# Kernel optimization log

Measured on AMD Instinct MI355X. Metric: run time of the kernel, lower is better.

The kernel has to match this reference:

```python
import jax, jax.numpy as jnp
import numpy as np

B, T, D, H, L, K, DFF = 8, 512, 512, 8, 4, 31, 2048
DK = D // H
PAD = (K - 1) // 2

def _ln(x, g, b, eps=1e-5):
    m = x.mean(-1, keepdims=True)
    v = ((x - m) ** 2).mean(-1, keepdims=True)
    return (x - m) * jax.lax.rsqrt(v + eps) * g + b

def _swish(x):
    return x * jax.nn.sigmoid(x)

def _rel_shift(x):
    # x: [B,H,T,P] with P = 2T-1 (Transformer-XL style shift)
    b, h, q, p = x.shape
    x = jnp.pad(x, ((0, 0), (0, 0), (0, 0), (1, 0)))
    x = x.reshape(b, h, p + 1, q)[:, :, 1:].reshape(b, h, q, p)
    return x

def setup_inputs() -> dict:
    key = jax.random.key(0)
    ks = iter(jax.random.split(key, 64))
    def w(shape, s=0.02):
        return jax.random.normal(next(ks), shape, jnp.float32) * s
    inp = {
        'x': jax.random.normal(next(ks), (B, T, D), jnp.float32),
        'pos_emb': jax.random.normal(next(ks), (1, 2 * T - 1, D), jnp.float32),
        'ln1_g': jnp.ones((L, D)), 'ln1_b': jnp.zeros((L, D)),
        'ff1_w1': w((L, D, DFF)), 'ff1_b1': jnp.zeros((L, DFF)),
        'ff1_w2': w((L, DFF, D)), 'ff1_b2': jnp.zeros((L, D)),
        'lnA_g': jnp.ones((L, D)), 'lnA_b': jnp.zeros((L, D)),
        'Wq': w((L, D, D)), 'bq': jnp.zeros((L, D)),
        'Wk': w((L, D, D)), 'bk': jnp.zeros((L, D)),
        'Wv': w((L, D, D)), 'bv': jnp.zeros((L, D)),
        'Wo': w((L, D, D)), 'bo': jnp.zeros((L, D)),
        'Wpos': w((L, D, D)),
        'pbu': jnp.zeros((L, H, DK)), 'pbv': jnp.zeros((L, H, DK)),
        'lnC_g': jnp.ones((L, D)), 'lnC_b': jnp.zeros((L, D)),
        'pw1_w': w((L, 2 * D, D)), 'pw1_b': jnp.zeros((L, 2 * D)),
        'dw_w': w((L, D, K)), 'dw_b': jnp.zeros((L, D)),
        'cln_g': jnp.ones((L, D)), 'cln_b': jnp.zeros((L, D)),
        'pw2_w': w((L, D, D)), 'pw2_b': jnp.zeros((L, D)),
        'ln2_g': jnp.ones((L, D)), 'ln2_b': jnp.zeros((L, D)),
        'ff2_w1': w((L, D, DFF)), 'ff2_b1': jnp.zeros((L, DFF)),
        'ff2_w2': w((L, DFF, D)), 'ff2_b2': jnp.zeros((L, D)),
        'lnO_g': jnp.ones((L, D)), 'lnO_b': jnp.zeros((L, D)),
    }
    return inp

def reference(x, pos_emb, ln1_g, ln1_b, ff1_w1, ff1_b1, ff1_w2, ff1_b2,
              lnA_g, lnA_b, Wq, bq, Wk, bk, Wv, bv, Wo, bo, Wpos, pbu, pbv,
              lnC_g, lnC_b, pw1_w, pw1_b, dw_w, dw_b, cln_g, cln_b, pw2_w, pw2_b,
              ln2_g, ln2_b, ff2_w1, ff2_b1, ff2_w2, ff2_b2, lnO_g, lnO_b):
    scale = 1.0 / np.sqrt(DK).astype(np.float32)
    for i in range(L):
        # FFN 1 (half-step residual)
        res = x
        y = _ln(x, ln1_g[i], ln1_b[i])
        y = _swish(y @ ff1_w1[i] + ff1_b1[i]) @ ff1_w2[i] + ff1_b2[i]
        res = res + 0.5 * y
        # rel-pos multi-head self-attention
        y = _ln(res, lnA_g[i], lnA_b[i])
        q = (y @ Wq[i] + bq[i]).reshape(B, T, H, DK)
        k = (y @ Wk[i] + bk[i]).reshape(B, T, H, DK)
        v = (y @ Wv[i] + bv[i]).reshape(B, T, H, DK)
        p = (pos_emb @ Wpos[i]).reshape(1, 2 * T - 1, H, DK)
        ac = jnp.einsum('bthd,bshd->bhts', q + pbu[i], k)          # content score
        bd = jnp.einsum('bthd,xshd->bhts', q + pbv[i], p)          # position score
        bd = _rel_shift(bd)[..., :T]
        attn = jax.nn.softmax((ac + bd) * scale, axis=-1)
        o = jnp.einsum('bhts,bshd->bthd', attn, v).reshape(B, T, D)
        res = res + (o @ Wo[i] + bo[i])
        # convolution module
        y = _ln(res, lnC_g[i], lnC_b[i])
        y = y @ pw1_w[i].T + pw1_b[i]                               # (B,T,2D)
        a, g = jnp.split(y, 2, axis=-1)
        y = a * jax.nn.sigmoid(g)                                   # GLU over channels
        y = jax.lax.conv_general_dilated(
            y.transpose(0, 2, 1), dw_w[i][:, None, :],
            window_strides=(1,), padding=[(PAD, PAD)],
            feature_group_count=D,
            dimension_numbers=('NCH', 'OIH', 'NCH'))
        y = y.transpose(0, 2, 1) + dw_b[i]                          # (B,T,D)
        y = _swish(_ln(y, cln_g[i], cln_b[i]))
        y = y @ pw2_w[i].T + pw2_b[i]
        res = res + y
        # FFN 2 (half-step residual)
        y = _ln(res, ln2_g[i], ln2_b[i])
        y = _swish(y @ ff2_w1[i] + ff2_b1[i]) @ ff2_w2[i] + ff2_b2[i]
        res = res + 0.5 * y
        x = _ln(res, lnO_g[i], lnO_b[i])
    return x
```

## Files before the change

kernel.cpp:

```cpp
#include <hip/hip_runtime.h>


typedef unsigned short u16;
typedef unsigned int u32;
typedef __attribute__((ext_vector_type(8))) short bf16x8;
typedef __attribute__((ext_vector_type(4))) float f32x4;

#define DI __device__ __forceinline__

constexpr int CT = 512;
constexpr int CD = 512;
constexpr int CH = 8;
constexpr int CDK = 64;
constexpr int CDFF = 2048;
constexpr int CNBT = 4096;
constexpr int CL = 4;

DI u16 f2bf(float f) {
  u32 u = __builtin_bit_cast(u32, f);
  u = u + 0x7fffu + ((u >> 16) & 1u);
  return (u16)(u >> 16);
}
DI float bf2f(u16 h) { u32 u = ((u32)h) << 16; return __builtin_bit_cast(float, u); }
DI u32 pack2(float a, float b) { return (u32)f2bf(a) | ((u32)f2bf(b) << 16); }
DI float sigm(float x) { return 1.0f / (1.0f + __expf(-x)); }

DI f32x4 MFMA(bf16x8 a, bf16x8 b, f32x4 c) {
  return __builtin_amdgcn_mfma_f32_16x16x32_bf16(a, b, c, 0, 0, 0);
}

DI void gload16(const void* g, void* l) {
  __builtin_amdgcn_global_load_lds((const __attribute__((address_space(1))) void*)g,
                                   (__attribute__((address_space(3))) void*)l, 16, 0, 0);
}

DI float wsum(float v) {
#pragma unroll
  for (int o = 32; o > 0; o >>= 1) v += __shfl_xor(v, o, 64);
  return v;
}

DI void tbody(const float* ip, u16* op, int R, int C, int c0, int r0,
              int tx, int ty) {
  __shared__ float t[32][33];
#pragma unroll
  for (int i = ty; i < 32; i += 8)
    t[i][tx] = ip[(long)(r0 + i) * C + c0 + tx];
  __syncthreads();
#pragma unroll
  for (int i = ty; i < 32; i += 8)
    op[(long)(c0 + i) * R + r0 + tx] = f2bf(t[tx][i]);
}

__global__ __launch_bounds__(256) void tconv2x_k(const float* __restrict__ in0,
                                                 const float* __restrict__ in1,
                                                 u16* __restrict__ out0,
                                                 u16* __restrict__ out1,
                                                 int R, int C) {
  int z = blockIdx.z;
  int l = z & 3;
  const float* ip = (z < 4 ? in0 : in1) + (long)l * R * C;
  u16* op = (z < 4 ? out0 : out1) + (long)l * R * C;
  tbody(ip, op, R, C, blockIdx.x * 32, blockIdx.y * 32, threadIdx.x, threadIdx.y);
}

__global__ __launch_bounds__(256) void tconvQ_k(
    const float* __restrict__ Wq, const float* __restrict__ Wk,
    const float* __restrict__ Wv, const float* __restrict__ Wo,
    const float* __restrict__ Wpos, u16* __restrict__ wt_qkv,
    u16* __restrict__ wt_o, u16* __restrict__ wt_pos) {
  int z = blockIdx.z;
  int sel = z >> 2, l = z & 3;
  const float* ip;
  u16* op;
  const long S = 512L * 512;
  switch (sel) {
    case 0: ip = Wq + l * S; op = wt_qkv + (long)l * 1536 * 512; break;
    case 1: ip = Wk + l * S; op = wt_qkv + (long)l * 1536 * 512 + S; break;
    case 2: ip = Wv + l * S; op = wt_qkv + (long)l * 1536 * 512 + 2 * S; break;
    case 3: ip = Wo + l * S; op = wt_o + l * S; break;
    default: ip = Wpos + l * S; op = wt_pos + l * S; break;
  }
  tbody(ip, op, 512, 512, blockIdx.x * 32, blockIdx.y * 32, threadIdx.x, threadIdx.y);
}

__global__ __launch_bounds__(256) void cvt_k(const float* __restrict__ in,
                                             u16* __restrict__ out, long nIn, long nOut,
                                             long inZ, long outZ) {
  long i = ((long)blockIdx.x * 256 + threadIdx.x) * 4;
  if (i >= nOut) return;
  const float* ip = in + (long)blockIdx.y * inZ;
  u16* op = out + (long)blockIdx.y * outZ;
  u16 o[4];
#pragma unroll
  for (int j = 0; j < 4; ++j) {
    long idx = i + j;
    o[j] = (idx < nIn) ? f2bf(ip[idx]) : (u16)0;
  }
  uint2 st;
  st.x = (u32)o[0] | ((u32)o[1] << 16);
  st.y = (u32)o[2] | ((u32)o[3] << 16);
  *(uint2*)&op[i] = st;
}

__global__ __launch_bounds__(256) void pwperm_k(const float* __restrict__ in,
                                                u16* __restrict__ out) {
  int l = blockIdx.y;
  long i = (long)blockIdx.x * 256 + threadIdx.x;
  long n = i >> 7;
  int c = (int)(i & 127) * 4;
  int q = (int)(n >> 4) & 1;
  long r = (q ? 512 : 0) + ((n >> 5) << 4) + (n & 15);
  const float* ip = in + ((long)l * 1024 + r) * 512 + c;
  float4 v = *(const float4*)ip;
  u16* op = out + ((long)l * 1024 + n) * 512 + c;
  uint2 st;
  st.x = pack2(v.x, v.y);
  st.y = pack2(v.z, v.w);
  *(uint2*)op = st;
}

__global__ __launch_bounds__(256) void dwt_k(const float* __restrict__ in,
                                             float* __restrict__ out) {
  int l = blockIdx.y;
  int idx = blockIdx.x * 256 + threadIdx.x;
  if (idx >= 512 * 31) return;
  int k = idx >> 9, d = idx & 511;
  out[(long)l * 31 * 512 + idx] = in[(long)l * 512 * 31 + d * 31 + k];
}

__global__ __launch_bounds__(256) void qkvbias_k(const float* __restrict__ bq,
                                                 const float* __restrict__ bk,
                                                 const float* __restrict__ bv,
                                                 float* __restrict__ out) {
  int z = blockIdx.y;
  int j = blockIdx.x * 256 + threadIdx.x;
  float v;
  if (j < 512) v = bq[z * 512 + j];
  else if (j < 1024) v = bk[z * 512 + j - 512];
  else v = bv[z * 512 + j - 1024];
  out[z * 1536 + j] = v;
}

__global__ __launch_bounds__(256) void copy_k(const float* __restrict__ in,
                                              float* __restrict__ out) {
  long i = ((long)blockIdx.x * 256 + threadIdx.x) * 4;
  *(float4*)(out + i) = *(const float4*)(in + i);
}

template <int F32OUT>
__global__ __launch_bounds__(256) void ln_k(const float* in, void* out,
                                            const float* gw, const float* bw) {
  int tid = threadIdx.x, wid = tid >> 6, lane = tid & 63;
  long row = (long)blockIdx.x * 4 + wid;
  const float* x = in + row * CD + lane * 8;
  float4 v0 = *(const float4*)x;
  float4 v1 = *(const float4*)(x + 4);
  float s = v0.x + v0.y + v0.z + v0.w + v1.x + v1.y + v1.z + v1.w;
  float q = v0.x * v0.x + v0.y * v0.y + v0.z * v0.z + v0.w * v0.w +
            v1.x * v1.x + v1.y * v1.y + v1.z * v1.z + v1.w * v1.w;
  s = wsum(s);
  q = wsum(q);
  float mean = s * (1.0f / CD);
  float var = q * (1.0f / CD) - mean * mean;
  float rs = rsqrtf(var + 1e-5f);
  int c = lane * 8;
  float4 g0 = *(const float4*)(gw + c), g1 = *(const float4*)(gw + c + 4);
  float4 b0 = *(const float4*)(bw + c), b1 = *(const float4*)(bw + c + 4);
  float y0 = (v0.x - mean) * rs * g0.x + b0.x;
  float y1 = (v0.y - mean) * rs * g0.y + b0.y;
  float y2 = (v0.z - mean) * rs * g0.z + b0.z;
  float y3 = (v0.w - mean) * rs * g0.w + b0.w;
  float y4 = (v1.x - mean) * rs * g1.x + b1.x;
  float y5 = (v1.y - mean) * rs * g1.y + b1.y;
  float y6 = (v1.z - mean) * rs * g1.z + b1.z;
  float y7 = (v1.w - mean) * rs * g1.w + b1.w;
  if (F32OUT) {
    float* o = (float*)out + row * CD + c;
    *(float4*)o = make_float4(y0, y1, y2, y3);
    *(float4*)(o + 4) = make_float4(y4, y5, y6, y7);
  } else {
    u16* o = (u16*)out + row * CD + c;
    uint4 pk;
    pk.x = pack2(y0, y1);
    pk.y = pack2(y2, y3);
    pk.z = pack2(y4, y5);
    pk.w = pack2(y6, y7);
    *(uint4*)o = pk;
  }
}

__global__ __launch_bounds__(256) void lnln_k(float* cur, u16* ybf,
                                              const float* gO, const float* bO,
                                              const float* g1, const float* b1) {
  int tid = threadIdx.x, wid = tid >> 6, lane = tid & 63;
  long row = (long)blockIdx.x * 4 + wid;
  float* x = cur + row * CD + lane * 8;
  float v[8];
  *(float4*)&v[0] = *(const float4*)x;
  *(float4*)&v[4] = *(const float4*)(x + 4);
  float s = 0.f, q = 0.f;
#pragma unroll
  for (int j = 0; j < 8; ++j) { s += v[j]; q += v[j] * v[j]; }
  s = wsum(s);
  q = wsum(q);
  float mean = s * (1.0f / CD);
  float var = q * (1.0f / CD) - mean * mean;
  float rs = rsqrtf(var + 1e-5f);
  int c = lane * 8;
  float y[8];
#pragma unroll
  for (int j = 0; j < 8; ++j) y[j] = (v[j] - mean) * rs * gO[c + j] + bO[c + j];
  *(float4*)x = *(float4*)&y[0];
  *(float4*)(x + 4) = *(float4*)&y[4];
  float s2 = 0.f, q2 = 0.f;
#pragma unroll
  for (int j = 0; j < 8; ++j) { s2 += y[j]; q2 += y[j] * y[j]; }
  s2 = wsum(s2);
  q2 = wsum(q2);
  float mean2 = s2 * (1.0f / CD);
  float var2 = q2 * (1.0f / CD) - mean2 * mean2;
  float rs2 = rsqrtf(var2 + 1e-5f);
  float z[8];
#pragma unroll
  for (int j = 0; j < 8; ++j) z[j] = (y[j] - mean2) * rs2 * g1[c + j] + b1[c + j];
  u16* o = ybf + row * CD + c;
  uint4 pk;
  pk.x = pack2(z[0], z[1]);
  pk.y = pack2(z[2], z[3]);
  pk.z = pack2(z[4], z[5]);
  pk.w = pack2(z[6], z[7]);
  *(uint4*)o = pk;
}

template <int EPI, int SPLITK>
__global__ __launch_bounds__(256, 2) void gemm2_k(
    const u16* __restrict__ A, const u16* __restrict__ B, void* C,
    u16* __restrict__ Caux,
    const float* __restrict__ bias, float alpha, int lda, int ldb, int ldc, int Kd) {
  __shared__ u16 lds[2][2][64 * 64];
  const int tid = threadIdx.x, wid = tid >> 6, lane = tid & 63;
  const int m0 = blockIdx.x * 64, n0 = blockIdx.y * 64;
  const int wm = wid >> 1, wn = wid & 1;
  const int fr = lane & 15, fq = lane >> 4;
  const f32x4 vz = {0.f, 0.f, 0.f, 0.f};
  f32x4 acc[2][2] = {{vz, vz}, {vz, vz}};

  const int Kc = Kd / SPLITK;
  const int kb0 = (SPLITK > 1) ? blockIdx.z * Kc : 0;
  const int nK = Kc / 64;

  auto stage = [&](int buf, int kt) {
    const int k0 = kb0 + kt * 64;
#pragma unroll
    for (int r = 0; r < 2; ++r) {
      int bi = r * 4096 + tid * 16;
      int row = bi >> 7;
      int ch = ((bi >> 4) & 7) ^ (row & 7);
      gload16(A + (long)(m0 + row) * lda + k0 + ch * 8,
              (char*)&lds[buf][0][0] + r * 4096 + wid * 1024);
      gload16(B + (long)(n0 + row) * ldb + k0 + ch * 8,
              (char*)&lds[buf][1][0] + r * 4096 + wid * 1024);
    }
  };

  stage(0, 0);
  asm volatile("s_waitcnt vmcnt(0)" ::: "memory");
  __syncthreads();
  int buf = 0;
  for (int kt = 0; kt < nK; ++kt) {
    if (kt + 1 < nK) stage(buf ^ 1, kt + 1);
    bf16x8 af[2][2], bfv[2][2];
#pragma unroll
    for (int ks = 0; ks < 2; ++ks) {
      int ch = ks * 4 + fq;
#pragma unroll
      for (int i = 0; i < 2; ++i) {
        int arow = wm * 32 + i * 16 + fr;
        af[ks][i] = *(const bf16x8*)((const char*)&lds[buf][0][0] + arow * 128 +
                                     ((ch ^ (arow & 7)) << 4));
        int brow = wn * 32 + i * 16 + fr;
        bfv[ks][i] = *(const bf16x8*)((const char*)&lds[buf][1][0] + brow * 128 +
                                      ((ch ^ (brow & 7)) << 4));
      }
    }
#pragma unroll
    for (int ks = 0; ks < 2; ++ks)
#pragma unroll
      for (int mi = 0; mi < 2; ++mi)
#pragma unroll
        for (int ni = 0; ni < 2; ++ni)
          acc[mi][ni] = MFMA(af[ks][mi], bfv[ks][ni], acc[mi][ni]);
    asm volatile("s_waitcnt vmcnt(0)" ::: "memory");
    __syncthreads();
    buf ^= 1;
  }

  if constexpr (EPI == 7) {
    const int ucol = (n0 >> 1) + wn * 16 + fr;
    float ba = bias[ucol], bg = bias[512 + ucol];
#pragma unroll
    for (int mi = 0; mi < 2; ++mi) {
      const int gmB = m0 + wm * 32 + mi * 16 + fq * 4;
#pragma unroll
      for (int r = 0; r < 4; ++r) {
        float va = acc[mi][0][r] + ba;
        float vg = acc[mi][1][r] + bg;
        ((u16*)C)[(long)(gmB + r) * 512 + ucol] = f2bf(va * sigm(vg));
      }
    }
  } else if constexpr (EPI == 8) {
    if (n0 < 1024) {
#pragma unroll
      for (int mi = 0; mi < 2; ++mi) {
        const int gmB = m0 + wm * 32 + mi * 16 + fq * 4;
#pragma unroll
        for (int ni = 0; ni < 2; ++ni) {
          const int gn = n0 + wn * 32 + ni * 16 + fr;
          float bv_ = bias[gn];
#pragma unroll
          for (int r = 0; r < 4; ++r)
            ((u16*)C)[(long)(gmB + r) * ldc + gn] = f2bf(acc[mi][ni][r] + bv_);
        }
      }
    } else {
#pragma unroll
      for (int mi = 0; mi < 2; ++mi) {
        const int gmB = m0 + wm * 32 + mi * 16 + fq * 4;
        const int b = gmB >> 9, t = gmB & 511;
#pragma unroll
        for (int ni = 0; ni < 2; ++ni) {
          const int gn = n0 + wn * 32 + ni * 16 + fr;
          const int h = (gn - 1024) >> 6, d = (gn - 1024) & 63;
          float bv_ = bias[gn];
          uint2 pk;
          pk.x = pack2(acc[mi][ni][0] + bv_, acc[mi][ni][1] + bv_);
          pk.y = pack2(acc[mi][ni][2] + bv_, acc[mi][ni][3] + bv_);
          *(uint2*)&Caux[((long)(b * 8 + h) * 64 + d) * 512 + t] = pk;
        }
      }
    }
  } else {
#pragma unroll
    for (int mi = 0; mi < 2; ++mi) {
      const int gmB = m0 + wm * 32 + mi * 16 + fq * 4;
#pragma unroll
      for (int ni = 0; ni < 2; ++ni) {
        const int gn = n0 + wn * 32 + ni * 16 + fr;
        float bv_ = 0.f;
        if constexpr (EPI == 1 || EPI == 2 || EPI == 3) bv_ = bias[gn];
#pragma unroll
        for (int r = 0; r < 4; ++r) {
          const int gm = gmB + r;
          float v = acc[mi][ni][r];
          long idx = (long)gm * ldc + gn;
          if constexpr (EPI == 0) ((u16*)C)[idx] = f2bf(v);
          else if constexpr (EPI == 1) ((u16*)C)[idx] = f2bf(v + bv_);
          else if constexpr (EPI == 2) {
            float x = v + bv_;
            ((u16*)C)[idx] = f2bf(x * sigm(x));
          } else if constexpr (EPI == 3) {
            float* R = (float*)C;
            if constexpr (SPLITK > 1) {
              float add = alpha * (v + (blockIdx.z == 0 ? bv_ : 0.f));
              atomicAdd(&R[idx], add);
            } else {
              R[idx] += alpha * (v + bv_);
            }
          }
        }
      }
    }
  }
}

__global__ __launch_bounds__(256, 2) void attn_k(
    const u16* __restrict__ qkvp, const u16* __restrict__ pball,
    const float* __restrict__ pbuL, const float* __restrict__ pbvL,
    const u16* __restrict__ vt, u16* __restrict__ out) {
  __shared__ u16 ldsK[2][64 * 64];
  __shared__ u16 ldsP[2][128 * 64];
  __shared__ u16 bd0s[4][16 * 80];
  __shared__ u16 stile[4][16 * 64];
  const int tid = threadIdx.x, wid = tid >> 6, lane = tid & 63;
  const int t0 = blockIdx.x * 64;
  const int bh = blockIdx.y, b = bh >> 3, h = bh & 7;
  const int fr = lane & 15, fq = lane >> 4;

  const u16* kbase = qkvp + (long)(b * CT) * 1536 + 512 + h * 64;
  const u16* pbase = pball + h * 64;
  const float* pu = pbuL + h * 64;
  const float* pv = pbvL + h * 64;

  const u16* qp = qkvp + (long)(b * CT + t0 + wid * 16 + fr) * 1536 + h * 64;
  bf16x8 qua[2], qva[2];
#pragma unroll
  for (int kk = 0; kk < 2; ++kk) {
    bf16x8 qw = *(const bf16x8*)(qp + kk * 32 + fq * 8);
    const float* bu = pu + kk * 32 + fq * 8;
    const float* bv = pv + kk * 32 + fq * 8;
#pragma unroll
    for (int j = 0; j < 8; ++j) {
      float qf = bf2f((u16)qw[j]);
      qua[kk][j] = (short)f2bf(qf + bu[j]);
      qva[kk][j] = (short)f2bf(qf + bv[j]);
    }
  }

  const f32x4 vz = {0.f, 0.f, 0.f, 0.f};
  f32x4 oacc[4] = {vz, vz, vz, vz};
  float m_run[4] = {-1e30f, -1e30f, -1e30f, -1e30f};
  float l_run[4] = {0.f, 0.f, 0.f, 0.f};
  const int jbw = (3 - wid) * 16;

  auto stage = [&](int buf, int st) {
    int s0 = st * 64, j0 = s0 - t0 + 448;
#pragma unroll
    for (int r = 0; r < 2; ++r) {
      int c = r * 256 + tid;
      int row = c >> 3, cs = (c & 7) ^ (row & 7);
      gload16(kbase + (long)(s0 + row) * 1536 + cs * 8,
              (char*)&ldsK[buf][0] + r * 4096 + wid * 1024);
    }
#pragma unroll
    for (int r = 0; r < 4; ++r) {
      int c = r * 256 + tid;
      int row = c >> 3, cs = (c & 7) ^ (row & 7);
      gload16(pbase + (long)(j0 + row) * 2048 + cs * 8,
              (char*)&ldsP[buf][0] + r * 4096 + wid * 1024);
    }
  };

  stage(0, 0);
  int cur = 0;
  for (int st = 0; st < 8; ++st) {
    const int s0 = st * 64;
    if (st + 1 < 8) {
      stage(cur ^ 1, st + 1);
      asm volatile("s_waitcnt vmcnt(6)" ::: "memory");
    } else {
      asm volatile("s_waitcnt vmcnt(0)" ::: "memory");
    }
    __syncthreads();

    bf16x8 vb[4][2];
#pragma unroll
    for (int ni = 0; ni < 4; ++ni)
#pragma unroll
      for (int kk = 0; kk < 2; ++kk)
        vb[ni][kk] = *(const bf16x8*)&vt[((long)bh * 64 + ni * 16 + fr) * 512 +
                                         s0 + kk * 32 + fq * 8];

    f32x4 ac[4] = {vz, vz, vz, vz};
#pragma unroll
    for (int kk = 0; kk < 2; ++kk) {
#pragma unroll
      for (int ni = 0; ni < 4; ++ni) {
        int row = ni * 16 + fr;
        bf16x8 kb = *(const bf16x8*)((const char*)&ldsK[cur][0] +
                                     ((row * 128 + kk * 64 + fq * 16) ^ ((row & 7) << 4)));
        ac[ni] = MFMA(qua[kk], kb, ac[ni]);
      }
    }
    f32x4 bd[5] = {vz, vz, vz, vz, vz};
#pragma unroll
    for (int kk = 0; kk < 2; ++kk) {
#pragma unroll
      for (int nbi = 0; nbi < 5; ++nbi) {
        int row = jbw + nbi * 16 + fr;
        bf16x8 pb = *(const bf16x8*)((const char*)&ldsP[cur][0] +
                                     ((row * 128 + kk * 64 + fq * 16) ^ ((row & 7) << 4)));
        bd[nbi] = MFMA(qva[kk], pb, bd[nbi]);
      }
    }
#pragma unroll
    for (int nbi = 0; nbi < 5; ++nbi)
#pragma unroll
      for (int r = 0; r < 4; ++r)
        bd0s[wid][(fq * 4 + r) * 80 + nbi * 16 + fr] = f2bf(bd[nbi][r]);

    float vals[4][4];
#pragma unroll
    for (int ni = 0; ni < 4; ++ni)
#pragma unroll
      for (int r = 0; r < 4; ++r) {
        int tlw = fq * 4 + r;
        int jcol = ni * 16 + fr + 15 - tlw;
        vals[ni][r] = (ac[ni][r] + bf2f(bd0s[wid][tlw * 80 + jcol])) * 0.125f;
      }
    float scf[4];
#pragma unroll
    for (int r = 0; r < 4; ++r) {
      float mx = fmaxf(fmaxf(vals[0][r], vals[1][r]), fmaxf(vals[2][r], vals[3][r]));
      mx = fmaxf(mx, __shfl_xor(mx, 1));
      mx = fmaxf(mx, __shfl_xor(mx, 2));
      mx = fmaxf(mx, __shfl_xor(mx, 4));
      mx = fmaxf(mx, __shfl_xor(mx, 8));
      float mnew = fmaxf(m_run[r], mx);
      scf[r] = __expf(m_run[r] - mnew);
      m_run[r] = mnew;
      float sum = 0.f;
#pragma unroll
      for (int ni = 0; ni < 4; ++ni) {
        float p = __expf(vals[ni][r] - mnew);
        vals[ni][r] = p;
        sum += p;
      }
      sum += __shfl_xor(sum, 1);
      sum += __shfl_xor(sum, 2);
      sum += __shfl_xor(sum, 4);
      sum += __shfl_xor(sum, 8);
      l_run[r] = l_run[r] * scf[r] + sum;
    }
#pragma unroll
    for (int ni = 0; ni < 4; ++ni)
#pragma unroll
      for (int r = 0; r < 4; ++r) {
        int tlw = fq * 4 + r;
        *(u16*)((char*)&stile[wid][0] +
                (((tlw * 128) + (ni * 16 + fr) * 2) ^ ((tlw & 7) << 4))) =
            f2bf(vals[ni][r]);
      }
#pragma unroll
    for (int ni = 0; ni < 4; ++ni)
#pragma unroll
      for (int r = 0; r < 4; ++r) oacc[ni][r] *= scf[r];
#pragma unroll
    for (int kk = 0; kk < 2; ++kk) {
      bf16x8 pa = *(const bf16x8*)((const char*)&stile[wid][0] +
                                   ((fr * 128 + kk * 64 + fq * 16) ^ ((fr & 7) << 4)));
#pragma unroll
      for (int ni = 0; ni < 4; ++ni) oacc[ni] = MFMA(pa, vb[ni][kk], oacc[ni]);
    }
    __syncthreads();
    cur ^= 1;
  }

  float inv[4];
#pragma unroll
  for (int r = 0; r < 4; ++r) inv[r] = 1.0f / l_run[r];
#pragma unroll
  for (int ni = 0; ni < 4; ++ni)
#pragma unroll
    for (int r = 0; r < 4; ++r) {
      long row = (long)(b * CT + t0 + wid * 16 + fq * 4 + r) * CD + h * CDK;
      out[row + ni * 16 + fr] = f2bf(oacc[ni][r] * inv[r]);
    }
}

__global__ __launch_bounds__(256) void conv2_k(const u16* __restrict__ u,
                                               const float* __restrict__ wT,
                                               const float* __restrict__ wb,
                                               const float* __restrict__ cg,
                                               const float* __restrict__ cb,
                                               u16* __restrict__ out) {
  constexpr int TT = 8;
  int tid = threadIdx.x, d0 = tid * 2;
  int b = blockIdx.y, t0 = blockIdx.x * TT;
  const u16* ub = u + ((long)b * CT) * CD + d0;

  u32 strip[TT + 30];
#pragma unroll
  for (int j = 0; j < TT + 30; ++j) {
    int tt = t0 + j - 15;
    strip[j] = ((unsigned)tt < (unsigned)CT) ? *(const u32*)(ub + (long)tt * CD) : 0u;
  }
  float2 bias = *(const float2*)(wb + d0);
  float a0[TT], a1[TT];
#pragma unroll
  for (int t = 0; t < TT; ++t) { a0[t] = bias.x; a1[t] = bias.y; }
#pragma unroll
  for (int k = 0; k < 31; ++k) {
    float2 wk = *(const float2*)(wT + k * CD + d0);
#pragma unroll
    for (int t = 0; t < TT; ++t) {
      u32 pr = strip[t + k];
      a0[t] += bf2f((u16)(pr & 0xffff)) * wk.x;
      a1[t] += bf2f((u16)(pr >> 16)) * wk.y;
    }
  }
  __shared__ float redS[4][TT], redQ[4][TT];
  int wid = tid >> 6, lane = tid & 63;
#pragma unroll
  for (int t = 0; t < TT; ++t) {
    float s = a0[t] + a1[t];
    float q = a0[t] * a0[t] + a1[t] * a1[t];
    s = wsum(s);
    q = wsum(q);
    if (lane == 0) { redS[wid][t] = s; redQ[wid][t] = q; }
  }
  __syncthreads();
  float2 g2 = *(const float2*)(cg + d0);
  float2 b2 = *(const float2*)(cb + d0);
#pragma unroll
  for (int t = 0; t < TT; ++t) {
    float s = redS[0][t] + redS[1][t] + redS[2][t] + redS[3][t];
    float q = redQ[0][t] + redQ[1][t] + redQ[2][t] + redQ[3][t];
    float mean = s * (1.f / 512), var = q * (1.f / 512) - mean * mean;
    float rs = rsqrtf(var + 1e-5f);
    float y0 = (a0[t] - mean) * rs * g2.x + b2.x;
    float y1 = (a1[t] - mean) * rs * g2.y + b2.y;
    y0 = y0 * sigm(y0);
    y1 = y1 * sigm(y1);
    *(u32*)(out + ((long)(b * CT + t0 + t)) * CD + d0) = pack2(y0, y1);
  }
}

extern "C" void kernel_launch(void* const* d_in, const int* in_sizes, int n_in,
                              void* d_out, int out_size, void* d_ws, size_t ws_size,
                              hipStream_t stream) {
  const float* in_x   = (const float*)d_in[0];
  const float* in_pos = (const float*)d_in[1];
  const float* ln1_g  = (const float*)d_in[2];
  const float* ln1_b  = (const float*)d_in[3];
  const float* ff1_w1 = (const float*)d_in[4];
  const float* ff1_b1 = (const float*)d_in[5];
  const float* ff1_w2 = (const float*)d_in[6];
  const float* ff1_b2 = (const float*)d_in[7];
  const float* lnA_g  = (const float*)d_in[8];
  const float* lnA_b  = (const float*)d_in[9];
  const float* Wq     = (const float*)d_in[10];
  const float* bq     = (const float*)d_in[11];
  const float* Wk     = (const float*)d_in[12];
  const float* bk     = (const float*)d_in[13];
  const float* Wv     = (const float*)d_in[14];
  const float* bv     = (const float*)d_in[15];
  const float* Wo     = (const float*)d_in[16];
  const float* bo     = (const float*)d_in[17];
  const float* Wpos   = (const float*)d_in[18];
  const float* pbu    = (const float*)d_in[19];
  const float* pbv    = (const float*)d_in[20];
  const float* lnC_g  = (const float*)d_in[21];
  const float* lnC_b  = (const float*)d_in[22];
  const float* pw1_w  = (const float*)d_in[23];
  const float* pw1_b  = (const float*)d_in[24];
  const float* dw_w   = (const float*)d_in[25];
  const float* dw_b   = (const float*)d_in[26];
  const float* cln_g  = (const float*)d_in[27];
  const float* cln_b  = (const float*)d_in[28];
  const float* pw2_w  = (const float*)d_in[29];
  const float* pw2_b  = (const float*)d_in[30];
  const float* ln2_g  = (const float*)d_in[31];
  const float* ln2_b  = (const float*)d_in[32];
  const float* ff2_w1 = (const float*)d_in[33];
  const float* ff2_b1 = (const float*)d_in[34];
  const float* ff2_w2 = (const float*)d_in[35];
  const float* ff2_b2 = (const float*)d_in[36];
  const float* lnO_g  = (const float*)d_in[37];
  const float* lnO_b  = (const float*)d_in[38];
  (void)in_sizes; (void)n_in; (void)out_size; (void)ws_size;

  char* ws = (char*)d_ws;
  size_t off = 0;
  auto alloc = [&](size_t bytes) -> void* {
    off = (off + 255) & ~(size_t)255;
    void* p = ws + off;
    off += bytes;
    return p;
  };

  u16* wt_ff1w1 = (u16*)alloc((size_t)CL * CDFF * CD * 2);
  u16* wt_ff1w2 = (u16*)alloc((size_t)CL * CD * CDFF * 2);
  u16* wt_qkv   = (u16*)alloc((size_t)CL * 1536 * CD * 2);
  u16* wt_o     = (u16*)alloc((size_t)CL * CD * CD * 2);
  u16* wt_pos   = (u16*)alloc((size_t)CL * CD * CD * 2);
  u16* w_pw1p   = (u16*)alloc((size_t)CL * 1024 * CD * 2);
  u16* w_pw2    = (u16*)alloc((size_t)CL * CD * CD * 2);
  u16* wt_ff2w1 = (u16*)alloc((size_t)CL * CDFF * CD * 2);
  u16* wt_ff2w2 = (u16*)alloc((size_t)CL * CD * CDFF * 2);
  float* qkvbias = (float*)alloc((size_t)CL * 1536 * 4);
  u16* posbf = (u16*)alloc((size_t)1024 * CD * 2);
  float* dwT = (float*)alloc((size_t)CL * 31 * CD * 4);
  u16* pbf_all = (u16*)alloc((size_t)1024 * 2048 * 2);
  float* cur = (float*)alloc((size_t)CNBT * CD * 4);
  u16* ybf   = (u16*)alloc((size_t)CNBT * CD * 2);
  u16* qkv   = (u16*)alloc((size_t)CNBT * 1536 * 2);
  u16* hbf   = (u16*)alloc((size_t)CNBT * CDFF * 2);
  u16* vt    = (u16*)alloc((size_t)64 * CDK * CT * 2);
  u16* obf   = (u16*)alloc((size_t)CNBT * CD * 2);
  u16* ubuf  = (u16*)alloc((size_t)CNBT * CD * 2);
  u16* cbf   = (u16*)alloc((size_t)CNBT * CD * 2);

  dim3 b256(256);
  dim3 tb(32, 8);

  tconv2x_k<<<dim3(CDFF / 32, CD / 32, 2 * CL), tb, 0, stream>>>(
      ff1_w1, ff2_w1, wt_ff1w1, wt_ff2w1, CD, CDFF);
  tconv2x_k<<<dim3(CD / 32, CDFF / 32, 2 * CL), tb, 0, stream>>>(
      ff1_w2, ff2_w2, wt_ff1w2, wt_ff2w2, CDFF, CD);
  tconvQ_k<<<dim3(CD / 32, CD / 32, 5 * CL), tb, 0, stream>>>(
      Wq, Wk, Wv, Wo, Wpos, wt_qkv, wt_o, wt_pos);
  pwperm_k<<<dim3(512, CL), b256, 0, stream>>>(pw1_w, w_pw1p);
  cvt_k<<<dim3(256, CL, 1), b256, 0, stream>>>(pw2_w, w_pw2, 512L * 512, 512L * 512,
                                               512L * 512, 512L * 512);
  cvt_k<<<dim3(512, 1, 1), b256, 0, stream>>>(in_pos, posbf, 1023L * 512, 1024L * 512, 0, 0);
  dwt_k<<<dim3(62, CL), b256, 0, stream>>>(dw_w, dwT);
  qkvbias_k<<<dim3(6, CL), b256, 0, stream>>>(bq, bk, bv, qkvbias);
  copy_k<<<dim3(2048), b256, 0, stream>>>(in_x, cur);
  gemm2_k<0, 1><<<dim3(16, 32, 1), b256, 0, stream>>>(
      posbf, wt_pos, pbf_all, nullptr, nullptr, 0.f, CD, CD, 2048, CD);
  ln_k<0><<<dim3(1024), b256, 0, stream>>>(cur, ybf, ln1_g, ln1_b);

  for (int i = 0; i < CL; ++i) {
    const u16* Wf1 = wt_ff1w1 + (long)i * CDFF * CD;
    const u16* Wf2 = wt_ff1w2 + (long)i * CD * CDFF;
    const u16* Wqk = wt_qkv + (long)i * 1536 * CD;
    const u16* Wou = wt_o + (long)i * CD * CD;
    const u16* Wp1 = w_pw1p + (long)i * 1024 * CD;
    const u16* Wp2 = w_pw2 + (long)i * CD * CD;
    const u16* Wf3 = wt_ff2w1 + (long)i * CDFF * CD;
    const u16* Wf4 = wt_ff2w2 + (long)i * CD * CDFF;

    gemm2_k<2, 1><<<dim3(64, 32, 1), b256, 0, stream>>>(
        ybf, Wf1, hbf, nullptr, ff1_b1 + (long)i * CDFF, 0.f, CD, CD, CDFF, CD);
    gemm2_k<3, 2><<<dim3(64, 8, 2), b256, 0, stream>>>(
        hbf, Wf2, cur, nullptr, ff1_b2 + i * CD, 0.5f, CDFF, CDFF, CD, CDFF);

    ln_k<0><<<dim3(1024), b256, 0, stream>>>(cur, ybf, lnA_g + i * CD, lnA_b + i * CD);
    gemm2_k<8, 1><<<dim3(64, 24, 1), b256, 0, stream>>>(
        ybf, Wqk, qkv, vt, qkvbias + i * 1536, 0.f, CD, CD, 1536, CD);
    attn_k<<<dim3(8, 64), b256, 0, stream>>>(qkv, pbf_all + i * 512, pbu + i * 512,
                                             pbv + i * 512, vt, obf);
    gemm2_k<3, 1><<<dim3(64, 8, 1), b256, 0, stream>>>(
        obf, Wou, cur, nullptr, bo + i * CD, 1.0f, CD, CD, CD, CD);

    ln_k<0><<<dim3(1024), b256, 0, stream>>>(cur, ybf, lnC_g + i * CD, lnC_b + i * CD);
    gemm2_k<7, 1><<<dim3(64, 16, 1), b256, 0, stream>>>(
        ybf, Wp1, ubuf, nullptr, pw1_b + (long)i * 1024, 0.f, CD, CD, 512, CD);
    conv2_k<<<dim3(CT / 8, 8), b256, 0, stream>>>(ubuf, dwT + (long)i * 31 * CD,
                                                  dw_b + i * CD, cln_g + i * CD,
                                                  cln_b + i * CD, cbf);
    gemm2_k<3, 1><<<dim3(64, 8, 1), b256, 0, stream>>>(
        cbf, Wp2, cur, nullptr, pw2_b + i * CD, 1.0f, CD, CD, CD, CD);

    ln_k<0><<<dim3(1024), b256, 0, stream>>>(cur, ybf, ln2_g + i * CD, ln2_b + i * CD);
    gemm2_k<2, 1><<<dim3(64, 32, 1), b256, 0, stream>>>(
        ybf, Wf3, hbf, nullptr, ff2_b1 + (long)i * CDFF, 0.f, CD, CD, CDFF, CD);
    gemm2_k<3, 2><<<dim3(64, 8, 2), b256, 0, stream>>>(
        hbf, Wf4, cur, nullptr, ff2_b2 + i * CD, 0.5f, CDFF, CDFF, CD, CDFF);

    if (i < CL - 1)
      lnln_k<<<dim3(1024), b256, 0, stream>>>(cur, ybf, lnO_g + i * CD, lnO_b + i * CD,
                                              ln1_g + (i + 1) * CD, ln1_b + (i + 1) * CD);
    else
      ln_k<1><<<dim3(1024), b256, 0, stream>>>(cur, d_out, lnO_g + i * CD, lnO_b + i * CD);
  }
}
```

Before: 794.8 us.

## Add 128x128-tile GEMM for wide projections and fuse setup kernels

Adds a gemmB_k kernel with 128x128 output tiles (each wave computing 4x4 MFMA fragments). It is used for the FFN up-projections, the fused QKV projection and the GLU pointwise conv, replacing the 64x64-tile GEMM there to get more operand reuse per LDS load and fewer blocks. The setup kernels (pos conversion, dw transpose, qkv bias) are merged into one launch, and the input copy is fused with the first layernorm. The larger tiles raise register and LDS pressure and cut the number of blocks, which may reduce occupancy and CU fill on the smaller GEMMs.

```diff
diff --git a/kernel.cpp b/kernel.cpp
--- a/kernel.cpp
+++ b/kernel.cpp
@@ -120,32 +120,45 @@
   *(uint2*)op = st;
 }
 
-__global__ __launch_bounds__(256) void dwt_k(const float* __restrict__ in,
-                                             float* __restrict__ out) {
-  int l = blockIdx.y;
-  int idx = blockIdx.x * 256 + threadIdx.x;
-  if (idx >= 512 * 31) return;
-  int k = idx >> 9, d = idx & 511;
-  out[(long)l * 31 * 512 + idx] = in[(long)l * 512 * 31 + d * 31 + k];
-}
-
-__global__ __launch_bounds__(256) void qkvbias_k(const float* __restrict__ bq,
-                                                 const float* __restrict__ bk,
-                                                 const float* __restrict__ bv,
-                                                 float* __restrict__ out) {
-  int z = blockIdx.y;
-  int j = blockIdx.x * 256 + threadIdx.x;
-  float v;
-  if (j < 512) v = bq[z * 512 + j];
-  else if (j < 1024) v = bk[z * 512 + j - 512];
-  else v = bv[z * 512 + j - 1024];
-  out[z * 1536 + j] = v;
-}
-
-__global__ __launch_bounds__(256) void copy_k(const float* __restrict__ in,
-                                              float* __restrict__ out) {
-  long i = ((long)blockIdx.x * 256 + threadIdx.x) * 4;
-  *(float4*)(out + i) = *(const float4*)(in + i);
+__global__ __launch_bounds__(256) void setup3_k(
+    const float* __restrict__ in_pos, u16* __restrict__ posbf,
+    const float* __restrict__ dw_w, float* __restrict__ dwT,
+    const float* __restrict__ bq, const float* __restrict__ bk,
+    const float* __restrict__ bv, float* __restrict__ qkvb) {
+  int y = blockIdx.y;
+  long x = blockIdx.x;
+  int tid = threadIdx.x;
+  if (y == 0) {
+    long i = (x * 256 + tid) * 4;
+    const long nIn = 1023L * 512, nOut = 1024L * 512;
+    if (i >= nOut) return;
+    u16 o[4];
+#pragma unroll
+    for (int j = 0; j < 4; ++j) {
+      long idx = i + j;
+      o[j] = (idx < nIn) ? f2bf(in_pos[idx]) : (u16)0;
+    }
+    uint2 st;
+    st.x = (u32)o[0] | ((u32)o[1] << 16);
+    st.y = (u32)o[2] | ((u32)o[3] << 16);
+    *(uint2*)&posbf[i] = st;
+  } else if (y == 1) {
+    long idx = x * 256 + tid;
+    if (idx >= 4L * 31 * 512) return;
+    long l = idx / (31 * 512);
+    int rem = (int)(idx % (31 * 512));
+    int k = rem >> 9, d = rem & 511;
+    dwT[idx] = dw_w[l * 512 * 31 + d * 31 + k];
+  } else {
+    long idx = x * 256 + tid;
+    if (idx >= 4L * 1536) return;
+    int z = (int)(idx / 1536), j = (int)(idx % 1536);
+    float v;
+    if (j < 512) v = bq[z * 512 + j];
+    else if (j < 1024) v = bk[z * 512 + j - 512];
+    else v = bv[z * 512 + j - 1024];
+    qkvb[idx] = v;
+  }
 }
 
 template <int F32OUT>
@@ -190,6 +203,40 @@
   }
 }
 
+__global__ __launch_bounds__(256) void ln_cp_k(const float* __restrict__ in,
+                                               float* __restrict__ cur,
+                                               u16* __restrict__ ybf,
+                                               const float* gw, const float* bw) {
+  int tid = threadIdx.x, wid = tid >> 6, lane = tid & 63;
+  long row = (long)blockIdx.x * 4 + wid;
+  const float* x = in + row * CD + lane * 8;
+  float v[8];
+  *(float4*)&v[0] = *(const float4*)x;
+  *(float4*)&v[4] = *(const float4*)(x + 4);
+  float* cx = cur + row * CD + lane * 8;
+  *(float4*)cx = *(float4*)&v[0];
+  *(float4*)(cx + 4) = *(float4*)&v[4];
+  float s = 0.f, q = 0.f;
+#pragma unroll
+  for (int j = 0; j < 8; ++j) { s += v[j]; q += v[j] * v[j]; }
+  s = wsum(s);
+  q = wsum(q);
+  float mean = s * (1.0f / CD);
+  float var = q * (1.0f / CD) - mean * mean;
+  float rs = rsqrtf(var + 1e-5f);
+  int c = lane * 8;
+  float y[8];
+#pragma unroll
+  for (int j = 0; j < 8; ++j) y[j] = (v[j] - mean) * rs * gw[c + j] + bw[c + j];
+  u16* o = ybf + row * CD + c;
+  uint4 pk;
+  pk.x = pack2(y[0], y[1]);
+  pk.y = pack2(y[2], y[3]);
+  pk.z = pack2(y[4], y[5]);
+  pk.w = pack2(y[6], y[7]);
+  *(uint4*)o = pk;
+}
+
 __global__ __launch_bounds__(256) void lnln_k(float* cur, u16* ybf,
                                               const float* gO, const float* bO,
                                               const float* g1, const float* b1) {
@@ -236,7 +283,6 @@
 template <int EPI, int SPLITK>
 __global__ __launch_bounds__(256, 2) void gemm2_k(
     const u16* __restrict__ A, const u16* __restrict__ B, void* C,
-    u16* __restrict__ Caux,
     const float* __restrict__ bias, float alpha, int lda, int ldb, int ldc, int Kd) {
   __shared__ u16 lds[2][2][64 * 64];
   const int tid = threadIdx.x, wid = tid >> 6, lane = tid & 63;
@@ -296,27 +342,136 @@
     buf ^= 1;
   }
 
-  if constexpr (EPI == 7) {
-    const int ucol = (n0 >> 1) + wn * 16 + fr;
-    float ba = bias[ucol], bg = bias[512 + ucol];
-#pragma unroll
-    for (int mi = 0; mi < 2; ++mi) {
-      const int gmB = m0 + wm * 32 + mi * 16 + fq * 4;
+#pragma unroll
+  for (int mi = 0; mi < 2; ++mi) {
+    const int gmB = m0 + wm * 32 + mi * 16 + fq * 4;
+#pragma unroll
+    for (int ni = 0; ni < 2; ++ni) {
+      const int gn = n0 + wn * 32 + ni * 16 + fr;
+      float bv_ = 0.f;
+      if constexpr (EPI == 3) bv_ = bias[gn];
 #pragma unroll
       for (int r = 0; r < 4; ++r) {
-        float va = acc[mi][0][r] + ba;
-        float vg = acc[mi][1][r] + bg;
-        ((u16*)C)[(long)(gmB + r) * 512 + ucol] = f2bf(va * sigm(vg));
+        const int gm = gmB + r;
+        float v = acc[mi][ni][r];
+        long idx = (long)gm * ldc + gn;
+        if constexpr (EPI == 0) ((u16*)C)[idx] = f2bf(v);
+        else if constexpr (EPI == 3) {
+          float* R = (float*)C;
+          if constexpr (SPLITK > 1) {
+            float add = alpha * (v + (blockIdx.z == 0 ? bv_ : 0.f));
+            atomicAdd(&R[idx], add);
+          } else {
+            R[idx] += alpha * (v + bv_);
+          }
+        }
+      }
+    }
+  }
+}
+
+template <int EPI>
+__global__ __launch_bounds__(256, 2) void gemmB_k(
+    const u16* __restrict__ A, const u16* __restrict__ B, void* C,
+    u16* __restrict__ Caux, const float* __restrict__ bias,
+    int lda, int ldb, int ldc, int Kd) {
+  __shared__ u16 ldsA[2][128 * 64];
+  __shared__ u16 ldsB[2][128 * 64];
+  const int tid = threadIdx.x, wid = tid >> 6, lane = tid & 63;
+  const int m0 = blockIdx.x * 128, n0 = blockIdx.y * 128;
+  const int wm = wid >> 1, wn = wid & 1;
+  const int fr = lane & 15, fq = lane >> 4;
+  const f32x4 vz = {0.f, 0.f, 0.f, 0.f};
+  f32x4 acc[4][4];
+#pragma unroll
+  for (int mi = 0; mi < 4; ++mi)
+#pragma unroll
+    for (int ni = 0; ni < 4; ++ni) acc[mi][ni] = vz;
+  const int nK = Kd / 64;
+
+  auto stage = [&](int buf, int kt) {
+    const int k0 = kt * 64;
+#pragma unroll
+    for (int r = 0; r < 4; ++r) {
+      int bi = r * 4096 + tid * 16;
+      int row = bi >> 7;
+      int ch = ((bi >> 4) & 7) ^ (row & 7);
+      gload16(A + (long)(m0 + row) * lda + k0 + ch * 8,
+              (char*)&ldsA[buf][0] + r * 4096 + wid * 1024);
+      gload16(B + (long)(n0 + row) * ldb + k0 + ch * 8,
+              (char*)&ldsB[buf][0] + r * 4096 + wid * 1024);
+    }
+  };
+
+  stage(0, 0);
+  asm volatile("s_waitcnt vmcnt(0)" ::: "memory");
+  __syncthreads();
+  int buf = 0;
+  for (int kt = 0; kt < nK; ++kt) {
+    if (kt + 1 < nK) stage(buf ^ 1, kt + 1);
+#pragma unroll
+    for (int ks = 0; ks < 2; ++ks) {
+      int ch = ks * 4 + fq;
+      bf16x8 af[4], bfv[4];
+#pragma unroll
+      for (int i = 0; i < 4; ++i) {
+        int arow = wm * 64 + i * 16 + fr;
+        af[i] = *(const bf16x8*)((const char*)&ldsA[buf][0] + arow * 128 +
+                                 ((ch ^ (arow & 7)) << 4));
+        int brow = wn * 64 + i * 16 + fr;
+        bfv[i] = *(const bf16x8*)((const char*)&ldsB[buf][0] + brow * 128 +
+                                  ((ch ^ (brow & 7)) << 4));
+      }
+#pragma unroll
+      for (int mi = 0; mi < 4; ++mi)
+#pragma unroll
+        for (int ni = 0; ni < 4; ++ni)
+          acc[mi][ni] = MFMA(af[mi], bfv[ni], acc[mi][ni]);
+    }
+    asm volatile("s_waitcnt vmcnt(0)" ::: "memory");
+    __syncthreads();
+    buf ^= 1;
+  }
+
+  if constexpr (EPI == 2) {
+#pragma unroll
+    for (int mi = 0; mi < 4; ++mi) {
+      const int gmB = m0 + wm * 64 + mi * 16 + fq * 4;
+#pragma unroll
+      for (int ni = 0; ni < 4; ++ni) {
+        const int gn = n0 + wn * 64 + ni * 16 + fr;
+        float bv_ = bias[gn];
+#pragma unroll
+        for (int r = 0; r < 4; ++r) {
+          float x = acc[mi][ni][r] + bv_;
+          ((u16*)C)[(long)(gmB + r) * ldc + gn] = f2bf(x * sigm(x));
+        }
+      }
+    }
+  } else if constexpr (EPI == 7) {
+#pragma unroll
+    for (int mi = 0; mi < 4; ++mi) {
+      const int gmB = m0 + wm * 64 + mi * 16 + fq * 4;
+#pragma unroll
+      for (int p = 0; p < 2; ++p) {
+        const int ucol = (n0 >> 1) + wn * 32 + p * 16 + fr;
+        float ba = bias[ucol], bg = bias[512 + ucol];
+#pragma unroll
+        for (int r = 0; r < 4; ++r) {
+          float va = acc[mi][2 * p][r] + ba;
+          float vg = acc[mi][2 * p + 1][r] + bg;
+          ((u16*)C)[(long)(gmB + r) * 512 + ucol] = f2bf(va * sigm(vg));
+        }
       }
     }
   } else if constexpr (EPI == 8) {
     if (n0 < 1024) {
 #pragma unroll
-      for (int mi = 0; mi < 2; ++mi) {
-        const int gmB = m0 + wm * 32 + mi * 16 + fq * 4;
-#pragma unroll
-        for (int ni = 0; ni < 2; ++ni) {
-          const int gn = n0 + wn * 32 + ni * 16 + fr;
+      for (int mi = 0; mi < 4; ++mi) {
+        const int gmB = m0 + wm * 64 + mi * 16 + fq * 4;
+#pragma unroll
+        for (int ni = 0; ni < 4; ++ni) {
+          const int gn = n0 + wn * 64 + ni * 16 + fr;
           float bv_ = bias[gn];
 #pragma unroll
           for (int r = 0; r < 4; ++r)
@@ -325,49 +480,18 @@
       }
     } else {
 #pragma unroll
-      for (int mi = 0; mi < 2; ++mi) {
-        const int gmB = m0 + wm * 32 + mi * 16 + fq * 4;
+      for (int mi = 0; mi < 4; ++mi) {
+        const int gmB = m0 + wm * 64 + mi * 16 + fq * 4;
         const int b = gmB >> 9, t = gmB & 511;
 #pragma unroll
-        for (int ni = 0; ni < 2; ++ni) {
-          const int gn = n0 + wn * 32 + ni * 16 + fr;
+        for (int ni = 0; ni < 4; ++ni) {
+          const int gn = n0 + wn * 64 + ni * 16 + fr;
           const int h = (gn - 1024) >> 6, d = (gn - 1024) & 63;
           float bv_ = bias[gn];
           uint2 pk;
           pk.x = pack2(acc[mi][ni][0] + bv_, acc[mi][ni][1] + bv_);
           pk.y = pack2(acc[mi][ni][2] + bv_, acc[mi][ni][3] + bv_);
           *(uint2*)&Caux[((long)(b * 8 + h) * 64 + d) * 512 + t] = pk;
-        }
-      }
-    }
-  } else {
-#pragma unroll
-    for (int mi = 0; mi < 2; ++mi) {
-      const int gmB = m0 + wm * 32 + mi * 16 + fq * 4;
-#pragma unroll
-      for (int ni = 0; ni < 2; ++ni) {
-        const int gn = n0 + wn * 32 + ni * 16 + fr;
-        float bv_ = 0.f;
-        if constexpr (EPI == 1 || EPI == 2 || EPI == 3) bv_ = bias[gn];
-#pragma unroll
-        for (int r = 0; r < 4; ++r) {
-          const int gm = gmB + r;
-          float v = acc[mi][ni][r];
-          long idx = (long)gm * ldc + gn;
-          if constexpr (EPI == 0) ((u16*)C)[idx] = f2bf(v);
-          else if constexpr (EPI == 1) ((u16*)C)[idx] = f2bf(v + bv_);
-          else if constexpr (EPI == 2) {
-            float x = v + bv_;
-            ((u16*)C)[idx] = f2bf(x * sigm(x));
-          } else if constexpr (EPI == 3) {
-            float* R = (float*)C;
-            if constexpr (SPLITK > 1) {
-              float add = alpha * (v + (blockIdx.z == 0 ? bv_ : 0.f));
-              atomicAdd(&R[idx], add);
-            } else {
-              R[idx] += alpha * (v + bv_);
-            }
-          }
         }
       }
     }
@@ -693,13 +817,11 @@
   pwperm_k<<<dim3(512, CL), b256, 0, stream>>>(pw1_w, w_pw1p);
   cvt_k<<<dim3(256, CL, 1), b256, 0, stream>>>(pw2_w, w_pw2, 512L * 512, 512L * 512,
                                                512L * 512, 512L * 512);
-  cvt_k<<<dim3(512, 1, 1), b256, 0, stream>>>(in_pos, posbf, 1023L * 512, 1024L * 512, 0, 0);
-  dwt_k<<<dim3(62, CL), b256, 0, stream>>>(dw_w, dwT);
-  qkvbias_k<<<dim3(6, CL), b256, 0, stream>>>(bq, bk, bv, qkvbias);
-  copy_k<<<dim3(2048), b256, 0, stream>>>(in_x, cur);
+  setup3_k<<<dim3(512, 3), b256, 0, stream>>>(in_pos, posbf, dw_w, dwT,
+                                              bq, bk, bv, qkvbias);
+  ln_cp_k<<<dim3(1024), b256, 0, stream>>>(in_x, cur, ybf, ln1_g, ln1_b);
   gemm2_k<0, 1><<<dim3(16, 32, 1), b256, 0, stream>>>(
-      posbf, wt_pos, pbf_all, nullptr, nullptr, 0.f, CD, CD, 2048, CD);
-  ln_k<0><<<dim3(1024), b256, 0, stream>>>(cur, ybf, ln1_g, ln1_b);
+      posbf, wt_pos, pbf_all, nullptr, 0.f, CD, CD, 2048, CD);
 
   for (int i = 0; i < CL; ++i) {
     const u16* Wf1 = wt_ff1w1 + (long)i * CDFF * CD;
@@ -711,33 +833,33 @@
     const u16* Wf3 = wt_ff2w1 + (long)i * CDFF * CD;
     const u16* Wf4 = wt_ff2w2 + (long)i * CD * CDFF;
 
-    gemm2_k<2, 1><<<dim3(64, 32, 1), b256, 0, stream>>>(
-        ybf, Wf1, hbf, nullptr, ff1_b1 + (long)i * CDFF, 0.f, CD, CD, CDFF, CD);
+    gemmB_k<2><<<dim3(32, 16, 1), b256, 0, stream>>>(
+        ybf, Wf1, hbf, nullptr, ff1_b1 + (long)i * CDFF, CD, CD, CDFF, CD);
     gemm2_k<3, 2><<<dim3(64, 8, 2), b256, 0, stream>>>(
-        hbf, Wf2, cur, nullptr, ff1_b2 + i * CD, 0.5f, CDFF, CDFF, CD, CDFF);
+        hbf, Wf2, cur, ff1_b2 + i * CD, 0.5f, CDFF, CDFF, CD, CDFF);
 
     ln_k<0><<<dim3(1024), b256, 0, stream>>>(cur, ybf, lnA_g + i * CD, lnA_b + i * CD);
-    gemm2_k<8, 1><<<dim3(64, 24, 1), b256, 0, stream>>>(
-        ybf, Wqk, qkv, vt, qkvbias + i * 1536, 0.f, CD, CD, 1536, CD);
+    gemmB_k<8><<<dim3(32, 12, 1), b256, 0, stream>>>(
+        ybf, Wqk, qkv, vt, qkvbias + i * 1536, CD, CD, 1536, CD);
     attn_k<<<dim3(8, 64), b256, 0, stream>>>(qkv, pbf_all + i * 512, pbu + i * 512,
                                              pbv + i * 512, vt, obf);
     gemm2_k<3, 1><<<dim3(64, 8, 1), b256, 0, stream>>>(
-        obf, Wou, cur, nullptr, bo + i * CD, 1.0f, CD, CD, CD, CD);
+        obf, Wou, cur, bo + i * CD, 1.0f, CD, CD, CD, CD);
 
     ln_k<0><<<dim3(1024), b256, 0, stream>>>(cur, ybf, lnC_g + i * CD, lnC_b + i * CD);
-    gemm2_k<7, 1><<<dim3(64, 16, 1), b256, 0, stream>>>(
-        ybf, Wp1, ubuf, nullptr, pw1_b + (long)i * 1024, 0.f, CD, CD, 512, CD);
+    gemmB_k<7><<<dim3(32, 8, 1), b256, 0, stream>>>(
+        ybf, Wp1, ubuf, nullptr, pw1_b + (long)i * 1024, CD, CD, 512, CD);
     conv2_k<<<dim3(CT / 8, 8), b256, 0, stream>>>(ubuf, dwT + (long)i * 31 * CD,
                                                   dw_b + i * CD, cln_g + i * CD,
                                                   cln_b + i * CD, cbf);
     gemm2_k<3, 1><<<dim3(64, 8, 1), b256, 0, stream>>>(
-        cbf, Wp2, cur, nullptr, pw2_b + i * CD, 1.0f, CD, CD, CD, CD);
+        cbf, Wp2, cur, pw2_b + i * CD, 1.0f, CD, CD, CD, CD);
 
     ln_k<0><<<dim3(1024), b256, 0, stream>>>(cur, ybf, ln2_g + i * CD, ln2_b + i * CD);
-    gemm2_k<2, 1><<<dim3(64, 32, 1), b256, 0, stream>>>(
-        ybf, Wf3, hbf, nullptr, ff2_b1 + (long)i * CDFF, 0.f, CD, CD, CDFF, CD);
+    gemmB_k<2><<<dim3(32, 16, 1), b256, 0, stream>>>(
+        ybf, Wf3, hbf, nullptr, ff2_b1 + (long)i * CDFF, CD, CD, CDFF, CD);
     gemm2_k<3, 2><<<dim3(64, 8, 2), b256, 0, stream>>>(
-        hbf, Wf4, cur, nullptr, ff2_b2 + i * CD, 0.5f, CDFF, CDFF, CD, CDFF);
+        hbf, Wf4, cur, ff2_b2 + i * CD, 0.5f, CDFF, CDFF, CD, CDFF);
 
     if (i < CL - 1)
       lnln_k<<<dim3(1024), b256, 0, stream>>>(cur, ybf, lnO_g + i * CD, lnO_b + i * CD,
```

Result: no change. 787.0 us (-1.0%).
